# Kernel tuning notes

Hardware: AMD Instinct MI355X
Metric: run time of the kernel (lower is better)

The kernel has to match this reference:

```python
import jax, jax.numpy as jnp
import numpy as np

N_NODES = 100000


def _gcn_layer(x, W, b, src, dst, n):
    # PyG GCNConv: x' = D^-1/2 (A+I) D^-1/2 (x W) + b, with self-loops added.
    x = x @ W  # [N, out]
    loop = jnp.arange(n, dtype=src.dtype)
    src_f = jnp.concatenate([src, loop])
    dst_f = jnp.concatenate([dst, loop])
    deg = jax.ops.segment_sum(jnp.ones_like(dst_f, dtype=x.dtype), dst_f, num_segments=n)
    dinv = jnp.where(deg > 0, jax.lax.rsqrt(deg), 0.0)
    norm = dinv[src_f] * dinv[dst_f]  # [E+N]
    msgs = x[src_f] * norm[:, None]   # gather + scale
    out = jax.ops.segment_sum(msgs, dst_f, num_segments=n)
    return out + b


def setup_inputs() -> dict:
    key = jax.random.key(0)
    ks = jax.random.split(key, 16)
    inputFeatures = jax.random.normal(ks[0], (N_NODES, 64), dtype=jnp.float32)
    edge_index = jax.random.randint(ks[1], (2, 1000000), 0, N_NODES, dtype=jnp.int64)

    def lin(k, fan_in, fan_out):
        s = 1.0 / np.sqrt(fan_in)
        return jax.random.uniform(k, (fan_in, fan_out), jnp.float32, -s, s)

    return {
        "inputFeatures": inputFeatures,
        "W1": lin(ks[2], 64, 100), "b1": jnp.zeros((100,), jnp.float32),
        "W2": lin(ks[3], 100, 50), "b2": jnp.zeros((50,), jnp.float32),
        "W3": lin(ks[4], 50, 25), "b3": jnp.zeros((25,), jnp.float32),
        "Wl1": lin(ks[5], 25, 25), "bl1": jnp.zeros((25,), jnp.float32),
        "Wl2": lin(ks[6], 25, 10), "bl2": jnp.zeros((10,), jnp.float32),
        "Wl3": lin(ks[7], 10, 1), "bl3": jnp.zeros((1,), jnp.float32),
        "edge_index": edge_index,
    }


def reference(inputFeatures, W1, b1, W2, b2, W3, b3, Wl1, bl1, Wl2, bl2, Wl3, bl3, edge_index):
    src, dst = edge_index[0], edge_index[1]
    n = inputFeatures.shape[0]
    x = jax.nn.relu(_gcn_layer(inputFeatures, W1, b1, src, dst, n))
    x = jax.nn.relu(_gcn_layer(x, W2, b2, src, dst, n))
    x = jax.nn.relu(_gcn_layer(x, W3, b3, src, dst, n))
    x = jax.nn.relu(x @ Wl1 + bl1)
    x = jax.nn.relu(x @ Wl2 + bl2)
    x = jax.nn.relu(x @ Wl3 + bl3)
    return x  # [N, 1]
```

## Files before the change

kernel.cpp:

```cpp
#include <hip/hip_runtime.h>
#include <hip/hip_fp16.h>
#include <cstdint>

constexpr int BSHIFT = 9;
constexpr int NBUCK  = 256;
constexpr int BUCKET_CAP = 6144;

struct alignas(16) H8 { __half2 a, b, c, d; };
struct alignas(8)  H4 { __half2 a, b; };

typedef _Float16 f16x8 __attribute__((ext_vector_type(8)));
typedef float    f32x4 __attribute__((ext_vector_type(4)));

__device__ __forceinline__ float4 add4(float4 a, float4 b) {
    return make_float4(a.x + b.x, a.y + b.y, a.z + b.z, a.w + b.w);
}
__device__ __forceinline__ float4 mul4s(float4 a, float s) {
    return make_float4(a.x * s, a.y * s, a.z * s, a.w * s);
}
__device__ __forceinline__ void acc_h8(float4& A0, float4& A1, const H8 v, float s) {
    float2 f0 = __half22float2(v.a), f1 = __half22float2(v.b);
    float2 f2 = __half22float2(v.c), f3 = __half22float2(v.d);
    A0.x = fmaf(f0.x, s, A0.x); A0.y = fmaf(f0.y, s, A0.y);
    A0.z = fmaf(f1.x, s, A0.z); A0.w = fmaf(f1.y, s, A0.w);
    A1.x = fmaf(f2.x, s, A1.x); A1.y = fmaf(f2.y, s, A1.y);
    A1.z = fmaf(f3.x, s, A1.z); A1.w = fmaf(f3.y, s, A1.w);
}


constexpr int EPT = 16;
__global__ __launch_bounds__(256) void partition_pack(
    const int* __restrict__ src, const int* __restrict__ dst,
    int* __restrict__ bucketCur, int* __restrict__ pairs, int ne, int nEdgeBlocks,
    const float* __restrict__ W1, const float* __restrict__ W2,
    const float* __restrict__ W3,
    __half* __restrict__ P1, __half* __restrict__ P2, __half* __restrict__ P3) {
    if (blockIdx.x == (unsigned)nEdgeBlocks) {
        int t = threadIdx.x;
        for (int i = t; i < 7 * 2 * 64 * 8; i += 256) {
            int j = i & 7, lane = (i >> 3) & 63, f = i >> 9;
            int mt = f >> 1, kf = f & 1;
            int k = kf * 32 + (lane >> 4) * 8 + j;
            int m = mt * 16 + (lane & 15);
            P1[i] = __float2half_rn(m < 100 ? W1[k * 100 + m] : 0.0f);
        }
        for (int i = t; i < 4 * 4 * 64 * 8; i += 256) {
            int j = i & 7, lane = (i >> 3) & 63, f = i >> 9;
            int mt = f >> 2, kf = f & 3;
            int k = kf * 32 + (lane >> 4) * 8 + j;
            int m = mt * 16 + (lane & 15);
            P2[i] = __float2half_rn((k < 100 && m < 50) ? W2[k * 50 + m] : 0.0f);
        }
        for (int i = t; i < 2 * 2 * 64 * 8; i += 256) {
            int j = i & 7, lane = (i >> 3) & 63, f = i >> 9;
            int mt = f >> 1, kf = f & 1;
            int k = kf * 32 + (lane >> 4) * 8 + j;
            int m = mt * 16 + (lane & 15);
            P3[i] = __float2half_rn((k < 50 && m < 25) ? W3[k * 25 + m] : 0.0f);
        }
        return;
    }
    __shared__ int lcnt[NBUCK];
    __shared__ int lbase[NBUCK];
    int base = blockIdx.x * (256 * EPT);
    if (threadIdx.x < NBUCK) lcnt[threadIdx.x] = 0;
    __syncthreads();
    int2 ed[EPT];
    int  rnk[EPT];
#pragma unroll
    for (int j = 0; j < EPT; ++j) {
        int e = base + j * 256 + threadIdx.x;
        if (e < ne) {
            int d = dst[e];
            ed[j] = make_int2(src[e], d);
            rnk[j] = atomicAdd(&lcnt[d >> BSHIFT], 1);
        } else {
            ed[j].y = -1;
        }
    }
    __syncthreads();
    if (threadIdx.x < NBUCK) {
        int c = lcnt[threadIdx.x];
        lbase[threadIdx.x] = c ? atomicAdd(&bucketCur[threadIdx.x], c) : 0;
    }
    __syncthreads();
#pragma unroll
    for (int j = 0; j < EPT; ++j) {
        if (ed[j].y >= 0) {
            int b = ed[j].y >> BSHIFT;
            int p = lbase[b] + rnk[j];
            if (p < BUCKET_CAP)
                pairs[(size_t)b * BUCKET_CAP + p] =
                    (ed[j].x << BSHIFT) | (ed[j].y & ((1 << BSHIFT) - 1));
        }
    }
}

__global__ __launch_bounds__(256) void bucket_csr_scan(
    const int* __restrict__ pairs, const int* __restrict__ bucketCnt,
    int* __restrict__ offs, float* __restrict__ dinv, int* __restrict__ csr,
    int n, int ne, int nbuckets) {
    constexpr int BN = 1 << BSHIFT;
    __shared__ int hist[BN];
    __shared__ int cur[BN];
    __shared__ int tmp[256];
    __shared__ int baseS;
    int b = blockIdx.x;
    int t = threadIdx.x;

    int c = (t < (unsigned)nbuckets) ? bucketCnt[t] : 0;
    tmp[t] = c;
    __syncthreads();
    for (int off = 1; off < 256; off <<= 1) {
        int v = (t >= (unsigned)off) ? tmp[t - off] : 0;
        __syncthreads();
        tmp[t] += v;
        __syncthreads();
    }
    if (t == 0) {
        baseS = b ? tmp[b - 1] : 0;
        if (b == 0) offs[n] = ne;
    }
    __syncthreads();
    int base = baseS;
    int cnt  = bucketCnt[b];
    const int* pb = pairs + (size_t)b * BUCKET_CAP;
    int nodeLo = b << BSHIFT;

    hist[t] = 0;
    hist[t + 256] = 0;
    __syncthreads();
    for (int e = t; e < cnt; e += 256)
        atomicAdd(&hist[pb[e] & (BN - 1)], 1);
    __syncthreads();

    int l0 = 2 * t, l1 = l0 + 1;
    int h0 = hist[l0], h1 = hist[l1];
    tmp[t] = h0 + h1;
    __syncthreads();
    for (int off = 1; off < 256; off <<= 1) {
        int v = (t >= (unsigned)off) ? tmp[t - off] : 0;
        __syncthreads();
        tmp[t] += v;
        __syncthreads();
    }
    int e0 = tmp[t] - (h0 + h1);
    int e1 = e0 + h0;
    int g0 = nodeLo + l0, g1 = nodeLo + l1;
    if (g0 < n) { offs[g0] = base + e0; dinv[g0] = rsqrtf((float)(h0 + 1)); }
    if (g1 < n) { offs[g1] = base + e1; dinv[g1] = rsqrtf((float)(h1 + 1)); }
    cur[l0] = e0;
    cur[l1] = e1;
    __syncthreads();

    for (int e = t; e < cnt; e += 256) {
        int p = pb[e];
        int pos = atomicAdd(&cur[p & (BN - 1)], 1);
        csr[base + pos] = ((unsigned)p) >> BSHIFT;
    }
}

__global__ void cvt_scale_f32_f16(const float* __restrict__ x, const float* __restrict__ dinv,
                                  __half* __restrict__ o, int n4) {
    int i = blockIdx.x * blockDim.x + threadIdx.x;
    if (i < n4) {
        float dv = dinv[i >> 4];
        float4 v = ((const float4*)x)[i];
        H4 h;
        h.a = __floats2half2_rn(v.x * dv, v.y * dv);
        h.b = __floats2half2_rn(v.z * dv, v.w * dv);
        ((H4*)o)[i] = h;
    }
}

constexpr int XSP = 72;
constexpr int HPS = 136;
__global__ __launch_bounds__(256, 4) void agg1gemm12(
    const __half* __restrict__ x, const int* __restrict__ offs,
    const int* __restrict__ csr, const float* __restrict__ dinv,
    const __half* __restrict__ P1, const float* __restrict__ b1,
    const __half* __restrict__ P2, __half* __restrict__ out, int n) {
    __shared__ alignas(16) _Float16 Xs[64 * XSP];
    __shared__ alignas(16) _Float16 Hs[64 * HPS];
    int tid = threadIdx.x, lane = tid & 63, w = tid >> 6;
    int lg = lane >> 4, lr = lane & 15;
    int blockBase = blockIdx.x * 64;

    for (int i = tid; i < 64 * 2; i += 256) {
        f16x8 zz = {};
        *(f16x8*)&Hs[(i >> 1) * HPS + 112 + (i & 1) * 8] = zz;
    }

    int f0 = (lane & 7) * 8;
#pragma unroll
    for (int p = 0; p < 2; ++p) {
        int nl = w * 16 + p * 8 + (lane >> 3);
        int node = blockBase + nl;
        float4 z4 = make_float4(0.f, 0.f, 0.f, 0.f);
        float4 a00 = z4, a01 = z4, a10 = z4, a11 = z4, a20 = z4, a21 = z4, a30 = z4, a31 = z4;
        float dv = 0.0f;
        if (node < n) {
            dv = dinv[node];
            H8 sv = *(const H8*)&x[(size_t)node * 64 + f0];
            acc_h8(a00, a01, sv, 1.0f);
            int e0 = offs[node], e1 = offs[node + 1];
            int e = e0;
            for (; e + 4 <= e1; e += 4) {
                int i0 = csr[e], i1 = csr[e + 1], i2 = csr[e + 2], i3 = csr[e + 3];
                H8 v0 = *(const H8*)&x[(size_t)i0 * 64 + f0];
                H8 v1 = *(const H8*)&x[(size_t)i1 * 64 + f0];
                H8 v2 = *(const H8*)&x[(size_t)i2 * 64 + f0];
                H8 v3 = *(const H8*)&x[(size_t)i3 * 64 + f0];
                acc_h8(a00, a01, v0, 1.0f);
                acc_h8(a10, a11, v1, 1.0f);
                acc_h8(a20, a21, v2, 1.0f);
                acc_h8(a30, a31, v3, 1.0f);
            }
            for (; e < e1; ++e) {
                H8 v = *(const H8*)&x[(size_t)csr[e] * 64 + f0];
                acc_h8(a00, a01, v, 1.0f);
            }
        }
        float4 A0 = add4(add4(a00, a10), add4(a20, a30));
        float4 A1 = add4(add4(a01, a11), add4(a21, a31));
        A0 = mul4s(A0, dv);
        A1 = mul4s(A1, dv);
        H8 h;
        h.a = __floats2half2_rn(A0.x, A0.y);
        h.b = __floats2half2_rn(A0.z, A0.w);
        h.c = __floats2half2_rn(A1.x, A1.y);
        h.d = __floats2half2_rn(A1.z, A1.w);
        *(H8*)&Xs[nl * XSP + f0] = h;
    }
    __syncthreads();

    const f16x8* P1v = (const f16x8*)P1;
    float b1v[7];
#pragma unroll
    for (int mt = 0; mt < 7; ++mt) {
        int m = mt * 16 + lr;
        b1v[mt] = (m < 100) ? b1[m] : 0.0f;
    }
    {
        int rowL = w * 16 + lr;
        f16x8 a0 = *(const f16x8*)&Xs[rowL * XSP + lg * 8];
        f16x8 a1 = *(const f16x8*)&Xs[rowL * XSP + 32 + lg * 8];
        int hbase = w * 16;
#pragma unroll
        for (int mt = 0; mt < 7; ++mt) {
            f16x8 w0 = P1v[(mt * 2 + 0) * 64 + lane];
            f16x8 w1 = P1v[(mt * 2 + 1) * 64 + lane];
            f32x4 acc = {};
            acc = __builtin_amdgcn_mfma_f32_16x16x32_f16(a0, w0, acc, 0, 0, 0);
            acc = __builtin_amdgcn_mfma_f32_16x16x32_f16(a1, w1, acc, 0, 0, 0);
            int col = mt * 16 + lr;
#pragma unroll
            for (int i = 0; i < 4; ++i) {
                int rloc = hbase + lg * 4 + i;
                Hs[rloc * HPS + col] = (_Float16)fmaxf(acc[i] + b1v[mt], 0.0f);
            }
        }
    }
    __syncthreads();

    const f16x8* P2v = (const f16x8*)P2;
#pragma unroll
    for (int mt = 0; mt < 4; ++mt) {
        f16x8 w0 = P2v[(mt * 4 + 0) * 64 + lane];
        f16x8 w1 = P2v[(mt * 4 + 1) * 64 + lane];
        f16x8 w2 = P2v[(mt * 4 + 2) * 64 + lane];
        f16x8 w3 = P2v[(mt * 4 + 3) * 64 + lane];
        int lbase = w * 16;
        const _Float16* hrow = &Hs[(size_t)(lbase + lr) * HPS];
        f16x8 a0 = *(const f16x8*)&hrow[lg * 8];
        f16x8 a1 = *(const f16x8*)&hrow[32 + lg * 8];
        f16x8 a2 = *(const f16x8*)&hrow[64 + lg * 8];
        f16x8 a3 = *(const f16x8*)&hrow[96 + lg * 8];
        f32x4 acc = {};
        acc = __builtin_amdgcn_mfma_f32_16x16x32_f16(a0, w0, acc, 0, 0, 0);
        acc = __builtin_amdgcn_mfma_f32_16x16x32_f16(a1, w1, acc, 0, 0, 0);
        acc = __builtin_amdgcn_mfma_f32_16x16x32_f16(a2, w2, acc, 0, 0, 0);
        acc = __builtin_amdgcn_mfma_f32_16x16x32_f16(a3, w3, acc, 0, 0, 0);
        int col = mt * 16 + lr;
#pragma unroll
        for (int i = 0; i < 4; ++i) {
            int node = blockBase + lbase + lg * 4 + i;
            if (node < n)
                out[(size_t)node * 64 + col] = __float2half_rn(acc[i] * dinv[node]);
        }
    }
}

constexpr int YP = 72;
__global__ __launch_bounds__(256) void agg2g3(
    const __half* __restrict__ s, const int* __restrict__ offs,
    const int* __restrict__ csr, const float* __restrict__ dinv,
    const float* __restrict__ b2, const __half* __restrict__ P3,
    __half* __restrict__ out, int n) {
    constexpr int MH = 50, SH = 64;
    __shared__ alignas(16) _Float16 Ys[32 * YP];
    int tid = threadIdx.x, lane = tid & 63, w = tid >> 6;
    int lg = lane >> 4, lr = lane & 15;
    int blockBase = blockIdx.x * 32;

    int nodeL = tid >> 3;
    int f0 = (tid & 7) * 8;
    int node = blockBase + nodeL;
    float v[8] = {0.f, 0.f, 0.f, 0.f, 0.f, 0.f, 0.f, 0.f};
    if (node < n && f0 < 56) {
        float dv = dinv[node];
        float4 z4 = make_float4(0.f, 0.f, 0.f, 0.f);
        float4 a00 = z4, a01 = z4, a10 = z4, a11 = z4, a20 = z4, a21 = z4, a30 = z4, a31 = z4;
        {
            H8 sv = *(const H8*)&s[(size_t)node * SH + f0];
            acc_h8(a00, a01, sv, 1.0f);
        }
        int e0 = offs[node], e1 = offs[node + 1];
        int e = e0;
        for (; e + 4 <= e1; e += 4) {
            int i0 = csr[e], i1 = csr[e + 1], i2 = csr[e + 2], i3 = csr[e + 3];
            H8 v0 = *(const H8*)&s[(size_t)i0 * SH + f0];
            H8 v1 = *(const H8*)&s[(size_t)i1 * SH + f0];
            H8 v2 = *(const H8*)&s[(size_t)i2 * SH + f0];
            H8 v3 = *(const H8*)&s[(size_t)i3 * SH + f0];
            acc_h8(a00, a01, v0, 1.0f);
            acc_h8(a10, a11, v1, 1.0f);
            acc_h8(a20, a21, v2, 1.0f);
            acc_h8(a30, a31, v3, 1.0f);
        }
        for (; e < e1; ++e) {
            H8 vv = *(const H8*)&s[(size_t)csr[e] * SH + f0];
            acc_h8(a00, a01, vv, 1.0f);
        }
        float4 A0 = add4(add4(a00, a10), add4(a20, a30));
        float4 A1 = add4(add4(a01, a11), add4(a21, a31));
        float vr[8] = {A0.x, A0.y, A0.z, A0.w, A1.x, A1.y, A1.z, A1.w};
#pragma unroll
        for (int i = 0; i < 8; ++i)
            v[i] = (f0 + i < MH) ? fmaxf(dv * vr[i] + b2[f0 + i], 0.0f) : 0.0f;
    }
    {
        H8 h;
        h.a = __floats2half2_rn(v[0], v[1]);
        h.b = __floats2half2_rn(v[2], v[3]);
        h.c = __floats2half2_rn(v[4], v[5]);
        h.d = __floats2half2_rn(v[6], v[7]);
        *(H8*)&Ys[nodeL * YP + f0] = h;
    }
    __syncthreads();

    int rt = w >> 1, mt = w & 1;
    const f16x8* P3v = (const f16x8*)P3;
    f16x8 w0 = P3v[(mt * 2 + 0) * 64 + lane];
    f16x8 w1 = P3v[(mt * 2 + 1) * 64 + lane];
    int rowL = rt * 16 + lr;
    f16x8 a0 = *(const f16x8*)&Ys[rowL * YP + lg * 8];
    f16x8 a1 = *(const f16x8*)&Ys[rowL * YP + 32 + lg * 8];
    f32x4 acc = {};
    acc = __builtin_amdgcn_mfma_f32_16x16x32_f16(a0, w0, acc, 0, 0, 0);
    acc = __builtin_amdgcn_mfma_f32_16x16x32_f16(a1, w1, acc, 0, 0, 0);
    int col = mt * 16 + lr;
#pragma unroll
    for (int i = 0; i < 4; ++i) {
        int nd = blockBase + rt * 16 + lg * 4 + i;
        if (nd < n)
            out[(size_t)nd * 32 + col] = __float2half_rn(acc[i] * dinv[nd]);
    }
}

__global__ __launch_bounds__(256) void agg3_mlp_h(
    const __half* __restrict__ s, const int* __restrict__ offs,
    const int* __restrict__ csr, const float* __restrict__ dinv,
    const float* __restrict__ bg,
    const float* __restrict__ Wl1, const float* __restrict__ bl1,
    const float* __restrict__ Wl2, const float* __restrict__ bl2,
    const float* __restrict__ Wl3, const float* __restrict__ bl3,
    float* __restrict__ out, int n) {
    constexpr int MH = 25, SH = 32, LPN = 4;
    __shared__ float W1s[625], W2s[250], W3s[10], b1s[25], b2s[10];
    __shared__ float accs[64 * 26];
    __shared__ float b3s;

    for (int i = threadIdx.x; i < 625; i += 256) W1s[i] = Wl1[i];
    for (int i = threadIdx.x; i < 250; i += 256) W2s[i] = Wl2[i];
    if (threadIdx.x < 10) { W3s[threadIdx.x] = Wl3[threadIdx.x]; b2s[threadIdx.x] = bl2[threadIdx.x]; }
    if (threadIdx.x < 25) b1s[threadIdx.x] = bl1[threadIdx.x];
    if (threadIdx.x == 0) b3s = bl3[0];

    int lane = threadIdx.x % LPN;
    int nl   = threadIdx.x / LPN;
    int node = blockIdx.x * 64 + nl;
    int f0 = lane * 8;

    if (node < n && f0 < MH) {
        float dv = dinv[node];
        float4 z = make_float4(0.f, 0.f, 0.f, 0.f);
        float4 a00 = z, a01 = z, a10 = z, a11 = z, a20 = z, a21 = z, a30 = z, a31 = z;
        {
            H8 sv = *(const H8*)&s[(size_t)node * SH + f0];
            acc_h8(a00, a01, sv, 1.0f);
        }
        int e0 = offs[node], e1 = offs[node + 1];
        int e = e0;
        for (; e + 4 <= e1; e += 4) {
            int i0 = csr[e], i1 = csr[e + 1], i2 = csr[e + 2], i3 = csr[e + 3];
            H8 v0 = *(const H8*)&s[(size_t)i0 * SH + f0];
            H8 v1 = *(const H8*)&s[(size_t)i1 * SH + f0];
            H8 v2 = *(const H8*)&s[(size_t)i2 * SH + f0];
            H8 v3 = *(const H8*)&s[(size_t)i3 * SH + f0];
            acc_h8(a00, a01, v0, 1.0f);
            acc_h8(a10, a11, v1, 1.0f);
            acc_h8(a20, a21, v2, 1.0f);
            acc_h8(a30, a31, v3, 1.0f);
        }
        for (; e < e1; ++e) {
            H8 v = *(const H8*)&s[(size_t)csr[e] * SH + f0];
            acc_h8(a00, a01, v, 1.0f);
        }
        float4 A0 = add4(add4(a00, a10), add4(a20, a30));
        float4 A1 = add4(add4(a01, a11), add4(a21, a31));
        float v[8] = {A0.x, A0.y, A0.z, A0.w, A1.x, A1.y, A1.z, A1.w};
#pragma unroll
        for (int i = 0; i < 8; ++i)
            if (f0 + i < MH)
                accs[nl * 26 + f0 + i] = fmaxf(dv * v[i] + bg[f0 + i], 0.0f);
    }
    __syncthreads();

    if (threadIdx.x < 64) {
        int nd = blockIdx.x * 64 + threadIdx.x;
        if (nd < n) {
            const float* xr = &accs[threadIdx.x * 26];
            float h1[25];
#pragma unroll
            for (int m = 0; m < 25; ++m) {
                float a = b1s[m];
#pragma unroll
                for (int k = 0; k < 25; ++k) a = fmaf(xr[k], W1s[k * 25 + m], a);
                h1[m] = fmaxf(a, 0.0f);
            }
            float h2[10];
#pragma unroll
            for (int m = 0; m < 10; ++m) {
                float a = b2s[m];
#pragma unroll
                for (int k = 0; k < 25; ++k) a = fmaf(h1[k], W2s[k * 10 + m], a);
                h2[m] = fmaxf(a, 0.0f);
            }
            float a = b3s;
#pragma unroll
            for (int k = 0; k < 10; ++k) a = fmaf(h2[k], W3s[k], a);
            out[nd] = fmaxf(a, 0.0f);
        }
    }
}


extern "C" void kernel_launch(void* const* d_in, const int* in_sizes, int n_in,
                              void* d_out, int out_size, void* d_ws, size_t ws_size,
                              hipStream_t stream) {
    const float* x0  = (const float*)d_in[0];
    const float* W1  = (const float*)d_in[1];
    const float* b1  = (const float*)d_in[2];
    const float* W2  = (const float*)d_in[3];
    const float* b2  = (const float*)d_in[4];
    const float* W3  = (const float*)d_in[5];
    const float* b3  = (const float*)d_in[6];
    const float* Wl1 = (const float*)d_in[7];
    const float* bl1 = (const float*)d_in[8];
    const float* Wl2 = (const float*)d_in[9];
    const float* bl2 = (const float*)d_in[10];
    const float* Wl3 = (const float*)d_in[11];
    const float* bl3 = (const float*)d_in[12];
    const int*   edge = (const int*)d_in[13];

    int n  = in_sizes[0] / 64;
    int ne = in_sizes[13] / 2;
    const int* esrc = edge;
    const int* edst = edge + ne;

    char* ws = (char*)d_ws;
    auto alloc = [&](size_t bytes) {
        char* p = ws;
        ws += (bytes + 255) & ~(size_t)255;
        return p;
    };
    int*    offs       = (int*)alloc((size_t)(n + 1) * 4);
    int*    bucketCur  = (int*)alloc(NBUCK * 4);
    int*    csr        = (int*)alloc((size_t)ne * 4);
    float*  dinv       = (float*)alloc((size_t)n * 4);
    __half* x0h        = (__half*)alloc((size_t)n * 64 * 2);
    __half* bufDh      = (__half*)alloc((size_t)n * 64 * 2);
    __half* bufCh      = (__half*)alloc((size_t)n * 32 * 2);
    __half* P1         = (__half*)alloc(7 * 2 * 64 * 8 * 2);
    __half* P2         = (__half*)alloc(4 * 4 * 64 * 8 * 2);
    __half* P3         = (__half*)alloc(2 * 2 * 64 * 8 * 2);
    int*    pairs = (int*)bufDh;
    (void)ws_size; (void)n_in; (void)out_size;

    int nbuckets = (n + (1 << BSHIFT) - 1) >> BSHIFT;
    int nchunk   = (ne + 256 * EPT - 1) / (256 * EPT);

    hipMemsetAsync(bucketCur, 0, NBUCK * 4, stream);
    partition_pack<<<nchunk + 1, 256, 0, stream>>>(
        esrc, edst, bucketCur, pairs, ne, nchunk, W1, W2, W3, P1, P2, P3);
    bucket_csr_scan<<<nbuckets, 256, 0, stream>>>(
        pairs, bucketCur, offs, dinv, csr, n, ne, nbuckets);

    cvt_scale_f32_f16<<<(n * 16 + 255) / 256, 256, 0, stream>>>(x0, dinv, x0h, n * 16);

    agg1gemm12<<<(n + 63) / 64, 256, 0, stream>>>(
        x0h, offs, csr, dinv, P1, b1, P2, bufDh, n);

    agg2g3<<<(n + 31) / 32, 256, 0, stream>>>(
        bufDh, offs, csr, dinv, b2, P3, bufCh, n);

    agg3_mlp_h<<<(n + 63) / 64, 256, 0, stream>>>(
        bufCh, offs, csr, dinv, b3, Wl1, bl1, Wl2, bl2, Wl3, bl3, (float*)d_out, n);
}
```

Baseline: 230.8 us.

## Fuse input fp16 conversion into CSR build and parallelize MLP head

```diff
diff --git a/kernel.cpp b/kernel.cpp
--- a/kernel.cpp
+++ b/kernel.cpp
@@ -5,6 +5,7 @@
 constexpr int BSHIFT = 9;
 constexpr int NBUCK  = 256;
 constexpr int BUCKET_CAP = 6144;
+constexpr int BN = 1 << BSHIFT;
 
 struct alignas(16) H8 { __half2 a, b, c, d; };
 struct alignas(8)  H4 { __half2 a, b; };
@@ -91,16 +92,16 @@
             int p = lbase[b] + rnk[j];
             if (p < BUCKET_CAP)
                 pairs[(size_t)b * BUCKET_CAP + p] =
-                    (ed[j].x << BSHIFT) | (ed[j].y & ((1 << BSHIFT) - 1));
-        }
-    }
-}
-
-__global__ __launch_bounds__(256) void bucket_csr_scan(
+                    (ed[j].x << BSHIFT) | (ed[j].y & (BN - 1));
+        }
+    }
+}
+
+__global__ __launch_bounds__(256) void bucket_csr_cvt(
     const int* __restrict__ pairs, const int* __restrict__ bucketCnt,
     int* __restrict__ offs, float* __restrict__ dinv, int* __restrict__ csr,
+    const float* __restrict__ x0, __half* __restrict__ x0h,
     int n, int ne, int nbuckets) {
-    constexpr int BN = 1 << BSHIFT;
     __shared__ int hist[BN];
     __shared__ int cur[BN];
     __shared__ int tmp[256];
@@ -147,8 +148,12 @@
     int e0 = tmp[t] - (h0 + h1);
     int e1 = e0 + h0;
     int g0 = nodeLo + l0, g1 = nodeLo + l1;
-    if (g0 < n) { offs[g0] = base + e0; dinv[g0] = rsqrtf((float)(h0 + 1)); }
-    if (g1 < n) { offs[g1] = base + e1; dinv[g1] = rsqrtf((float)(h1 + 1)); }
+    float dv0 = rsqrtf((float)(h0 + 1));
+    float dv1 = rsqrtf((float)(h1 + 1));
+    if (g0 < n) { offs[g0] = base + e0; dinv[g0] = dv0; }
+    if (g1 < n) { offs[g1] = base + e1; dinv[g1] = dv1; }
+    hist[l0] = __float_as_int(dv0);
+    hist[l1] = __float_as_int(dv1);
     cur[l0] = e0;
     cur[l1] = e1;
     __syncthreads();
@@ -158,18 +163,20 @@
         int pos = atomicAdd(&cur[p & (BN - 1)], 1);
         csr[base + pos] = ((unsigned)p) >> BSHIFT;
     }
-}
-
-__global__ void cvt_scale_f32_f16(const float* __restrict__ x, const float* __restrict__ dinv,
-                                  __half* __restrict__ o, int n4) {
-    int i = blockIdx.x * blockDim.x + threadIdx.x;
-    if (i < n4) {
-        float dv = dinv[i >> 4];
-        float4 v = ((const float4*)x)[i];
+    __syncthreads();
+
+    int nloc = n - nodeLo;
+    if (nloc > BN) nloc = BN;
+    int cnt16 = nloc * 16;
+    for (int i = t; i < cnt16; i += 256) {
+        int r = i >> 4;
+        float dv = __int_as_float(hist[r]);
+        size_t gi = (size_t)(nodeLo + r) * 16 + (i & 15);
+        float4 v = ((const float4*)x0)[gi];
         H4 h;
         h.a = __floats2half2_rn(v.x * dv, v.y * dv);
         h.b = __floats2half2_rn(v.z * dv, v.w * dv);
-        ((H4*)o)[i] = h;
+        ((H4*)x0h)[gi] = h;
     }
 }
 
@@ -297,7 +304,6 @@
     const int* __restrict__ csr, const float* __restrict__ dinv,
     const float* __restrict__ b2, const __half* __restrict__ P3,
     __half* __restrict__ out, int n) {
-    constexpr int MH = 50, SH = 64;
     __shared__ alignas(16) _Float16 Ys[32 * YP];
     int tid = threadIdx.x, lane = tid & 63, w = tid >> 6;
     int lg = lane >> 4, lr = lane & 15;
@@ -312,24 +318,24 @@
         float4 z4 = make_float4(0.f, 0.f, 0.f, 0.f);
         float4 a00 = z4, a01 = z4, a10 = z4, a11 = z4, a20 = z4, a21 = z4, a30 = z4, a31 = z4;
         {
-            H8 sv = *(const H8*)&s[(size_t)node * SH + f0];
+            H8 sv = *(const H8*)&s[(size_t)node * 64 + f0];
             acc_h8(a00, a01, sv, 1.0f);
         }
         int e0 = offs[node], e1 = offs[node + 1];
         int e = e0;
         for (; e + 4 <= e1; e += 4) {
             int i0 = csr[e], i1 = csr[e + 1], i2 = csr[e + 2], i3 = csr[e + 3];
-            H8 v0 = *(const H8*)&s[(size_t)i0 * SH + f0];
-            H8 v1 = *(const H8*)&s[(size_t)i1 * SH + f0];
-            H8 v2 = *(const H8*)&s[(size_t)i2 * SH + f0];
-            H8 v3 = *(const H8*)&s[(size_t)i3 * SH + f0];
+            H8 v0 = *(const H8*)&s[(size_t)i0 * 64 + f0];
+            H8 v1 = *(const H8*)&s[(size_t)i1 * 64 + f0];
+            H8 v2 = *(const H8*)&s[(size_t)i2 * 64 + f0];
+            H8 v3 = *(const H8*)&s[(size_t)i3 * 64 + f0];
             acc_h8(a00, a01, v0, 1.0f);
             acc_h8(a10, a11, v1, 1.0f);
             acc_h8(a20, a21, v2, 1.0f);
             acc_h8(a30, a31, v3, 1.0f);
         }
         for (; e < e1; ++e) {
-            H8 vv = *(const H8*)&s[(size_t)csr[e] * SH + f0];
+            H8 vv = *(const H8*)&s[(size_t)csr[e] * 64 + f0];
             acc_h8(a00, a01, vv, 1.0f);
         }
         float4 A0 = add4(add4(a00, a10), add4(a20, a30));
@@ -337,7 +343,7 @@
         float vr[8] = {A0.x, A0.y, A0.z, A0.w, A1.x, A1.y, A1.z, A1.w};
 #pragma unroll
         for (int i = 0; i < 8; ++i)
-            v[i] = (f0 + i < MH) ? fmaxf(dv * vr[i] + b2[f0 + i], 0.0f) : 0.0f;
+            v[i] = (f0 + i < 50) ? fmaxf(dv * vr[i] + b2[f0 + i], 0.0f) : 0.0f;
     }
     {
         H8 h;
@@ -376,9 +382,10 @@
     const float* __restrict__ Wl2, const float* __restrict__ bl2,
     const float* __restrict__ Wl3, const float* __restrict__ bl3,
     float* __restrict__ out, int n) {
-    constexpr int MH = 25, SH = 32, LPN = 4;
     __shared__ float W1s[625], W2s[250], W3s[10], b1s[25], b2s[10];
     __shared__ float accs[64 * 26];
+    __shared__ float h1s[64 * 25];
+    __shared__ float h2s[64 * 12];
     __shared__ float b3s;
 
     for (int i = threadIdx.x; i < 625; i += 256) W1s[i] = Wl1[i];
@@ -387,34 +394,34 @@
     if (threadIdx.x < 25) b1s[threadIdx.x] = bl1[threadIdx.x];
     if (threadIdx.x == 0) b3s = bl3[0];
 
-    int lane = threadIdx.x % LPN;
-    int nl   = threadIdx.x / LPN;
+    int lane = threadIdx.x & 3;
+    int nl   = threadIdx.x >> 2;
     int node = blockIdx.x * 64 + nl;
     int f0 = lane * 8;
 
-    if (node < n && f0 < MH) {
+    if (node < n && f0 < 25) {
         float dv = dinv[node];
-        float4 z = make_float4(0.f, 0.f, 0.f, 0.f);
-        float4 a00 = z, a01 = z, a10 = z, a11 = z, a20 = z, a21 = z, a30 = z, a31 = z;
+        float4 z4 = make_float4(0.f, 0.f, 0.f, 0.f);
+        float4 a00 = z4, a01 = z4, a10 = z4, a11 = z4, a20 = z4, a21 = z4, a30 = z4, a31 = z4;
         {
-            H8 sv = *(const H8*)&s[(size_t)node * SH + f0];
+            H8 sv = *(const H8*)&s[(size_t)node * 32 + f0];
             acc_h8(a00, a01, sv, 1.0f);
         }
         int e0 = offs[node], e1 = offs[node + 1];
         int e = e0;
         for (; e + 4 <= e1; e += 4) {
             int i0 = csr[e], i1 = csr[e + 1], i2 = csr[e + 2], i3 = csr[e + 3];
-            H8 v0 = *(const H8*)&s[(size_t)i0 * SH + f0];
-            H8 v1 = *(const H8*)&s[(size_t)i1 * SH + f0];
-            H8 v2 = *(const H8*)&s[(size_t)i2 * SH + f0];
-            H8 v3 = *(const H8*)&s[(size_t)i3 * SH + f0];
+            H8 v0 = *(const H8*)&s[(size_t)i0 * 32 + f0];
+            H8 v1 = *(const H8*)&s[(size_t)i1 * 32 + f0];
+            H8 v2 = *(const H8*)&s[(size_t)i2 * 32 + f0];
+            H8 v3 = *(const H8*)&s[(size_t)i3 * 32 + f0];
             acc_h8(a00, a01, v0, 1.0f);
             acc_h8(a10, a11, v1, 1.0f);
             acc_h8(a20, a21, v2, 1.0f);
             acc_h8(a30, a31, v3, 1.0f);
         }
         for (; e < e1; ++e) {
-            H8 v = *(const H8*)&s[(size_t)csr[e] * SH + f0];
+            H8 v = *(const H8*)&s[(size_t)csr[e] * 32 + f0];
             acc_h8(a00, a01, v, 1.0f);
         }
         float4 A0 = add4(add4(a00, a10), add4(a20, a30));
@@ -422,36 +429,39 @@
         float v[8] = {A0.x, A0.y, A0.z, A0.w, A1.x, A1.y, A1.z, A1.w};
 #pragma unroll
         for (int i = 0; i < 8; ++i)
-            if (f0 + i < MH)
+            if (f0 + i < 25)
                 accs[nl * 26 + f0 + i] = fmaxf(dv * v[i] + bg[f0 + i], 0.0f);
     }
     __syncthreads();
 
-    if (threadIdx.x < 64) {
-        int nd = blockIdx.x * 64 + threadIdx.x;
-        if (nd < n) {
-            const float* xr = &accs[threadIdx.x * 26];
-            float h1[25];
-#pragma unroll
-            for (int m = 0; m < 25; ++m) {
-                float a = b1s[m];
-#pragma unroll
-                for (int k = 0; k < 25; ++k) a = fmaf(xr[k], W1s[k * 25 + m], a);
-                h1[m] = fmaxf(a, 0.0f);
-            }
-            float h2[10];
-#pragma unroll
-            for (int m = 0; m < 10; ++m) {
-                float a = b2s[m];
-#pragma unroll
-                for (int k = 0; k < 25; ++k) a = fmaf(h1[k], W2s[k * 10 + m], a);
-                h2[m] = fmaxf(a, 0.0f);
-            }
-            float a = b3s;
-#pragma unroll
-            for (int k = 0; k < 10; ++k) a = fmaf(h2[k], W3s[k], a);
-            out[nd] = fmaxf(a, 0.0f);
-        }
+    if (node < n) {
+        const float* xr = &accs[nl * 26];
+        for (int m = lane; m < 25; m += 4) {
+            float acc = b1s[m];
+#pragma unroll
+            for (int k = 0; k < 25; ++k) acc = fmaf(xr[k], W1s[k * 25 + m], acc);
+            h1s[nl * 25 + m] = fmaxf(acc, 0.0f);
+        }
+    }
+    __syncthreads();
+
+    if (node < n) {
+        const float* hr = &h1s[nl * 25];
+        for (int m = lane; m < 10; m += 4) {
+            float acc = b2s[m];
+#pragma unroll
+            for (int k = 0; k < 25; ++k) acc = fmaf(hr[k], W2s[k * 10 + m], acc);
+            h2s[nl * 12 + m] = fmaxf(acc, 0.0f);
+        }
+    }
+    __syncthreads();
+
+    if (node < n && lane == 0) {
+        const float* h2 = &h2s[nl * 12];
+        float acc = b3s;
+#pragma unroll
+        for (int k = 0; k < 10; ++k) acc = fmaf(h2[k], W3s[k], acc);
+        out[node] = fmaxf(acc, 0.0f);
     }
 }
 
@@ -504,10 +514,8 @@
     hipMemsetAsync(bucketCur, 0, NBUCK * 4, stream);
     partition_pack<<<nchunk + 1, 256, 0, stream>>>(
         esrc, edst, bucketCur, pairs, ne, nchunk, W1, W2, W3, P1, P2, P3);
-    bucket_csr_scan<<<nbuckets, 256, 0, stream>>>(
-        pairs, bucketCur, offs, dinv, csr, n, ne, nbuckets);
-
-    cvt_scale_f32_f16<<<(n * 16 + 255) / 256, 256, 0, stream>>>(x0, dinv, x0h, n * 16);
+    bucket_csr_cvt<<<nbuckets, 256, 0, stream>>>(
+        pairs, bucketCur, offs, dinv, csr, x0, x0h, n, ne, nbuckets);
 
     agg1gemm12<<<(n + 63) / 64, 256, 0, stream>>>(
         x0h, offs, csr, dinv, P1, b1, P2, bufDh, n);
```

After: 238.9 us. +3.5%, slower.

## Sort nodes by in-degree into a permutation to balance aggregation warps

Applied to the files above, without the earlier changes.

```diff
diff --git a/kernel.cpp b/kernel.cpp
--- a/kernel.cpp
+++ b/kernel.cpp
@@ -5,6 +5,7 @@
 constexpr int BSHIFT = 9;
 constexpr int NBUCK  = 256;
 constexpr int BUCKET_CAP = 6144;
+constexpr int BN = 1 << BSHIFT;
 
 struct alignas(16) H8 { __half2 a, b, c, d; };
 struct alignas(8)  H4 { __half2 a, b; };
@@ -91,7 +92,7 @@
             int p = lbase[b] + rnk[j];
             if (p < BUCKET_CAP)
                 pairs[(size_t)b * BUCKET_CAP + p] =
-                    (ed[j].x << BSHIFT) | (ed[j].y & ((1 << BSHIFT) - 1));
+                    (ed[j].x << BSHIFT) | (ed[j].y & (BN - 1));
         }
     }
 }
@@ -99,11 +100,11 @@
 __global__ __launch_bounds__(256) void bucket_csr_scan(
     const int* __restrict__ pairs, const int* __restrict__ bucketCnt,
     int* __restrict__ offs, float* __restrict__ dinv, int* __restrict__ csr,
-    int n, int ne, int nbuckets) {
-    constexpr int BN = 1 << BSHIFT;
+    int* __restrict__ binCount, int n, int ne, int nbuckets) {
     __shared__ int hist[BN];
     __shared__ int cur[BN];
     __shared__ int tmp[256];
+    __shared__ int binLoc[64];
     __shared__ int baseS;
     int b = blockIdx.x;
     int t = threadIdx.x;
@@ -136,6 +137,7 @@
 
     int l0 = 2 * t, l1 = l0 + 1;
     int h0 = hist[l0], h1 = hist[l1];
+    if (t < 64) binLoc[t] = 0;
     tmp[t] = h0 + h1;
     __syncthreads();
     for (int off = 1; off < 256; off <<= 1) {
@@ -147,17 +149,49 @@
     int e0 = tmp[t] - (h0 + h1);
     int e1 = e0 + h0;
     int g0 = nodeLo + l0, g1 = nodeLo + l1;
-    if (g0 < n) { offs[g0] = base + e0; dinv[g0] = rsqrtf((float)(h0 + 1)); }
-    if (g1 < n) { offs[g1] = base + e1; dinv[g1] = rsqrtf((float)(h1 + 1)); }
+    if (g0 < n) {
+        offs[g0] = base + e0; dinv[g0] = rsqrtf((float)(h0 + 1));
+        atomicAdd(&binLoc[h0 < 63 ? h0 : 63], 1);
+    }
+    if (g1 < n) {
+        offs[g1] = base + e1; dinv[g1] = rsqrtf((float)(h1 + 1));
+        atomicAdd(&binLoc[h1 < 63 ? h1 : 63], 1);
+    }
     cur[l0] = e0;
     cur[l1] = e1;
     __syncthreads();
+    if (t < 64 && binLoc[t]) atomicAdd(&binCount[t], binLoc[t]);
 
     for (int e = t; e < cnt; e += 256) {
         int p = pb[e];
         int pos = atomicAdd(&cur[p & (BN - 1)], 1);
         csr[base + pos] = ((unsigned)p) >> BSHIFT;
     }
+}
+
+__global__ __launch_bounds__(256) void build_perm(
+    const int* __restrict__ offs, const int* __restrict__ binCount,
+    int* __restrict__ binNext, int* __restrict__ perm, int n) {
+    __shared__ int binBase[64];
+    __shared__ int binLoc[64];
+    __shared__ int binResv[64];
+    int b = blockIdx.x, t = threadIdx.x;
+    if (t == 0) {
+        int s = 0;
+        for (int i = 0; i < 64; ++i) { binBase[i] = s; s += binCount[i]; }
+    }
+    if (t < 64) binLoc[t] = 0;
+    __syncthreads();
+    int nodeLo = b << BSHIFT;
+    int g0 = nodeLo + 2 * t, g1 = g0 + 1;
+    int d0 = 0, d1 = 0, r0 = 0, r1 = 0;
+    if (g0 < n) { int d = offs[g0 + 1] - offs[g0]; d0 = d < 63 ? d : 63; r0 = atomicAdd(&binLoc[d0], 1); }
+    if (g1 < n) { int d = offs[g1 + 1] - offs[g1]; d1 = d < 63 ? d : 63; r1 = atomicAdd(&binLoc[d1], 1); }
+    __syncthreads();
+    if (t < 64) binResv[t] = binLoc[t] ? atomicAdd(&binNext[t], binLoc[t]) : 0;
+    __syncthreads();
+    if (g0 < n) perm[binBase[d0] + binResv[d0] + r0] = g0;
+    if (g1 < n) perm[binBase[d1] + binResv[d1] + r1] = g1;
 }
 
 __global__ void cvt_scale_f32_f16(const float* __restrict__ x, const float* __restrict__ dinv,
@@ -178,10 +212,12 @@
 __global__ __launch_bounds__(256, 4) void agg1gemm12(
     const __half* __restrict__ x, const int* __restrict__ offs,
     const int* __restrict__ csr, const float* __restrict__ dinv,
+    const int* __restrict__ perm,
     const __half* __restrict__ P1, const float* __restrict__ b1,
     const __half* __restrict__ P2, __half* __restrict__ out, int n) {
     __shared__ alignas(16) _Float16 Xs[64 * XSP];
     __shared__ alignas(16) _Float16 Hs[64 * HPS];
+    __shared__ int permS[64];
     int tid = threadIdx.x, lane = tid & 63, w = tid >> 6;
     int lg = lane >> 4, lr = lane & 15;
     int blockBase = blockIdx.x * 64;
@@ -190,16 +226,21 @@
         f16x8 zz = {};
         *(f16x8*)&Hs[(i >> 1) * HPS + 112 + (i & 1) * 8] = zz;
     }
+    if (tid < 64) {
+        int idx = blockBase + tid;
+        permS[tid] = (idx < n) ? perm[idx] : -1;
+    }
+    __syncthreads();
 
     int f0 = (lane & 7) * 8;
 #pragma unroll
     for (int p = 0; p < 2; ++p) {
         int nl = w * 16 + p * 8 + (lane >> 3);
-        int node = blockBase + nl;
+        int node = permS[nl];
         float4 z4 = make_float4(0.f, 0.f, 0.f, 0.f);
         float4 a00 = z4, a01 = z4, a10 = z4, a11 = z4, a20 = z4, a21 = z4, a30 = z4, a31 = z4;
         float dv = 0.0f;
-        if (node < n) {
+        if (node >= 0) {
             dv = dinv[node];
             H8 sv = *(const H8*)&x[(size_t)node * 64 + f0];
             acc_h8(a00, a01, sv, 1.0f);
@@ -284,8 +325,8 @@
         int col = mt * 16 + lr;
 #pragma unroll
         for (int i = 0; i < 4; ++i) {
-            int node = blockBase + lbase + lg * 4 + i;
-            if (node < n)
+            int node = permS[lbase + lg * 4 + i];
+            if (node >= 0)
                 out[(size_t)node * 64 + col] = __float2half_rn(acc[i] * dinv[node]);
         }
     }
@@ -295,41 +336,48 @@
 __global__ __launch_bounds__(256) void agg2g3(
     const __half* __restrict__ s, const int* __restrict__ offs,
     const int* __restrict__ csr, const float* __restrict__ dinv,
+    const int* __restrict__ perm,
     const float* __restrict__ b2, const __half* __restrict__ P3,
     __half* __restrict__ out, int n) {
-    constexpr int MH = 50, SH = 64;
     __shared__ alignas(16) _Float16 Ys[32 * YP];
+    __shared__ int permS[32];
     int tid = threadIdx.x, lane = tid & 63, w = tid >> 6;
     int lg = lane >> 4, lr = lane & 15;
     int blockBase = blockIdx.x * 32;
 
+    if (tid < 32) {
+        int idx = blockBase + tid;
+        permS[tid] = (idx < n) ? perm[idx] : -1;
+    }
+    __syncthreads();
+
     int nodeL = tid >> 3;
     int f0 = (tid & 7) * 8;
-    int node = blockBase + nodeL;
+    int node = permS[nodeL];
     float v[8] = {0.f, 0.f, 0.f, 0.f, 0.f, 0.f, 0.f, 0.f};
-    if (node < n && f0 < 56) {
+    if (node >= 0 && f0 < 56) {
         float dv = dinv[node];
         float4 z4 = make_float4(0.f, 0.f, 0.f, 0.f);
         float4 a00 = z4, a01 = z4, a10 = z4, a11 = z4, a20 = z4, a21 = z4, a30 = z4, a31 = z4;
         {
-            H8 sv = *(const H8*)&s[(size_t)node * SH + f0];
+            H8 sv = *(const H8*)&s[(size_t)node * 64 + f0];
             acc_h8(a00, a01, sv, 1.0f);
         }
         int e0 = offs[node], e1 = offs[node + 1];
         int e = e0;
         for (; e + 4 <= e1; e += 4) {
             int i0 = csr[e], i1 = csr[e + 1], i2 = csr[e + 2], i3 = csr[e + 3];
-            H8 v0 = *(const H8*)&s[(size_t)i0 * SH + f0];
-            H8 v1 = *(const H8*)&s[(size_t)i1 * SH + f0];
-            H8 v2 = *(const H8*)&s[(size_t)i2 * SH + f0];
-            H8 v3 = *(const H8*)&s[(size_t)i3 * SH + f0];
+            H8 v0 = *(const H8*)&s[(size_t)i0 * 64 + f0];
+            H8 v1 = *(const H8*)&s[(size_t)i1 * 64 + f0];
+            H8 v2 = *(const H8*)&s[(size_t)i2 * 64 + f0];
+            H8 v3 = *(const H8*)&s[(size_t)i3 * 64 + f0];
             acc_h8(a00, a01, v0, 1.0f);
             acc_h8(a10, a11, v1, 1.0f);
             acc_h8(a20, a21, v2, 1.0f);
             acc_h8(a30, a31, v3, 1.0f);
         }
         for (; e < e1; ++e) {
-            H8 vv = *(const H8*)&s[(size_t)csr[e] * SH + f0];
+            H8 vv = *(const H8*)&s[(size_t)csr[e] * 64 + f0];
             acc_h8(a00, a01, vv, 1.0f);
         }
         float4 A0 = add4(add4(a00, a10), add4(a20, a30));
@@ -337,7 +385,7 @@
         float vr[8] = {A0.x, A0.y, A0.z, A0.w, A1.x, A1.y, A1.z, A1.w};
 #pragma unroll
         for (int i = 0; i < 8; ++i)
-            v[i] = (f0 + i < MH) ? fmaxf(dv * vr[i] + b2[f0 + i], 0.0f) : 0.0f;
+            v[i] = (f0 + i < 50) ? fmaxf(dv * vr[i] + b2[f0 + i], 0.0f) : 0.0f;
     }
     {
         H8 h;
@@ -362,8 +410,8 @@
     int col = mt * 16 + lr;
 #pragma unroll
     for (int i = 0; i < 4; ++i) {
-        int nd = blockBase + rt * 16 + lg * 4 + i;
-        if (nd < n)
+        int nd = permS[rt * 16 + lg * 4 + i];
+        if (nd >= 0)
             out[(size_t)nd * 32 + col] = __float2half_rn(acc[i] * dinv[nd]);
     }
 }
@@ -371,14 +419,16 @@
 __global__ __launch_bounds__(256) void agg3_mlp_h(
     const __half* __restrict__ s, const int* __restrict__ offs,
     const int* __restrict__ csr, const float* __restrict__ dinv,
+    const int* __restrict__ perm,
     const float* __restrict__ bg,
     const float* __restrict__ Wl1, const float* __restrict__ bl1,
     const float* __restrict__ Wl2, const float* __restrict__ bl2,
     const float* __restrict__ Wl3, const float* __restrict__ bl3,
     float* __restrict__ out, int n) {
-    constexpr int MH = 25, SH = 32, LPN = 4;
+    constexpr int LPN = 4;
     __shared__ float W1s[625], W2s[250], W3s[10], b1s[25], b2s[10];
     __shared__ float accs[64 * 26];
+    __shared__ int permS[64];
     __shared__ float b3s;
 
     for (int i = threadIdx.x; i < 625; i += 256) W1s[i] = Wl1[i];
@@ -386,35 +436,40 @@
     if (threadIdx.x < 10) { W3s[threadIdx.x] = Wl3[threadIdx.x]; b2s[threadIdx.x] = bl2[threadIdx.x]; }
     if (threadIdx.x < 25) b1s[threadIdx.x] = bl1[threadIdx.x];
     if (threadIdx.x == 0) b3s = bl3[0];
+    if (threadIdx.x < 64) {
+        int idx = blockIdx.x * 64 + threadIdx.x;
+        permS[threadIdx.x] = (idx < n) ? perm[idx] : -1;
+    }
+    __syncthreads();
 
     int lane = threadIdx.x % LPN;
     int nl   = threadIdx.x / LPN;
-    int node = blockIdx.x * 64 + nl;
+    int node = permS[nl];
     int f0 = lane * 8;
 
-    if (node < n && f0 < MH) {
+    if (node >= 0 && f0 < 25) {
         float dv = dinv[node];
-        float4 z = make_float4(0.f, 0.f, 0.f, 0.f);
-        float4 a00 = z, a01 = z, a10 = z, a11 = z, a20 = z, a21 = z, a30 = z, a31 = z;
+        float4 z4 = make_float4(0.f, 0.f, 0.f, 0.f);
+        float4 a00 = z4, a01 = z4, a10 = z4, a11 = z4, a20 = z4, a21 = z4, a30 = z4, a31 = z4;
         {
-            H8 sv = *(const H8*)&s[(size_t)node * SH + f0];
+            H8 sv = *(const H8*)&s[(size_t)node * 32 + f0];
             acc_h8(a00, a01, sv, 1.0f);
         }
         int e0 = offs[node], e1 = offs[node + 1];
         int e = e0;
         for (; e + 4 <= e1; e += 4) {
             int i0 = csr[e], i1 = csr[e + 1], i2 = csr[e + 2], i3 = csr[e + 3];
-            H8 v0 = *(const H8*)&s[(size_t)i0 * SH + f0];
-            H8 v1 = *(const H8*)&s[(size_t)i1 * SH + f0];
-            H8 v2 = *(const H8*)&s[(size_t)i2 * SH + f0];
-            H8 v3 = *(const H8*)&s[(size_t)i3 * SH + f0];
+            H8 v0 = *(const H8*)&s[(size_t)i0 * 32 + f0];
+            H8 v1 = *(const H8*)&s[(size_t)i1 * 32 + f0];
+            H8 v2 = *(const H8*)&s[(size_t)i2 * 32 + f0];
+            H8 v3 = *(const H8*)&s[(size_t)i3 * 32 + f0];
             acc_h8(a00, a01, v0, 1.0f);
             acc_h8(a10, a11, v1, 1.0f);
             acc_h8(a20, a21, v2, 1.0f);
             acc_h8(a30, a31, v3, 1.0f);
         }
         for (; e < e1; ++e) {
-            H8 v = *(const H8*)&s[(size_t)csr[e] * SH + f0];
+            H8 v = *(const H8*)&s[(size_t)csr[e] * 32 + f0];
             acc_h8(a00, a01, v, 1.0f);
         }
         float4 A0 = add4(add4(a00, a10), add4(a20, a30));
@@ -422,14 +477,14 @@
         float v[8] = {A0.x, A0.y, A0.z, A0.w, A1.x, A1.y, A1.z, A1.w};
 #pragma unroll
         for (int i = 0; i < 8; ++i)
-            if (f0 + i < MH)
+            if (f0 + i < 25)
                 accs[nl * 26 + f0 + i] = fmaxf(dv * v[i] + bg[f0 + i], 0.0f);
     }
     __syncthreads();
 
     if (threadIdx.x < 64) {
-        int nd = blockIdx.x * 64 + threadIdx.x;
-        if (nd < n) {
+        int nd = permS[threadIdx.x];
+        if (nd >= 0) {
             const float* xr = &accs[threadIdx.x * 26];
             float h1[25];
 #pragma unroll
@@ -486,35 +541,40 @@
         return p;
     };
     int*    offs       = (int*)alloc((size_t)(n + 1) * 4);
-    int*    bucketCur  = (int*)alloc(NBUCK * 4);
+    int*    bucketCur  = (int*)alloc((NBUCK + 128) * 4);
     int*    csr        = (int*)alloc((size_t)ne * 4);
     float*  dinv       = (float*)alloc((size_t)n * 4);
+    int*    perm       = (int*)alloc((size_t)n * 4);
     __half* x0h        = (__half*)alloc((size_t)n * 64 * 2);
     __half* bufDh      = (__half*)alloc((size_t)n * 64 * 2);
     __half* bufCh      = (__half*)alloc((size_t)n * 32 * 2);
     __half* P1         = (__half*)alloc(7 * 2 * 64 * 8 * 2);
     __half* P2         = (__half*)alloc(4 * 4 * 64 * 8 * 2);
     __half* P3         = (__half*)alloc(2 * 2 * 64 * 8 * 2);
+    int* binCount = bucketCur + NBUCK;
+    int* binNext  = bucketCur + NBUCK + 64;
     int*    pairs = (int*)bufDh;
     (void)ws_size; (void)n_in; (void)out_size;
 
     int nbuckets = (n + (1 << BSHIFT) - 1) >> BSHIFT;
     int nchunk   = (ne + 256 * EPT - 1) / (256 * EPT);
 
-    hipMemsetAsync(bucketCur, 0, NBUCK * 4, stream);
+    hipMemsetAsync(bucketCur, 0, (NBUCK + 128) * 4, stream);
     partition_pack<<<nchunk + 1, 256, 0, stream>>>(
         esrc, edst, bucketCur, pairs, ne, nchunk, W1, W2, W3, P1, P2, P3);
     bucket_csr_scan<<<nbuckets, 256, 0, stream>>>(
-        pairs, bucketCur, offs, dinv, csr, n, ne, nbuckets);
+        pairs, bucketCur, offs, dinv, csr, binCount, n, ne, nbuckets);
+
+    build_perm<<<nbuckets, 256, 0, stream>>>(offs, binCount, binNext, perm, n);
 
     cvt_scale_f32_f16<<<(n * 16 + 255) / 256, 256, 0, stream>>>(x0, dinv, x0h, n * 16);
 
     agg1gemm12<<<(n + 63) / 64, 256, 0, stream>>>(
-        x0h, offs, csr, dinv, P1, b1, P2, bufDh, n);
+        x0h, offs, csr, dinv, perm, P1, b1, P2, bufDh, n);
 
     agg2g3<<<(n + 31) / 32, 256, 0, stream>>>(
-        bufDh, offs, csr, dinv, b2, P3, bufCh, n);
+        bufDh, offs, csr, dinv, perm, b2, P3, bufCh, n);
 
     agg3_mlp_h<<<(n + 63) / 64, 256, 0, stream>>>(
-        bufCh, offs, csr, dinv, b3, Wl1, bl1, Wl2, bl2, Wl3, bl3, (float*)d_out, n);
-}
+        bufCh, offs, csr, dinv, perm, b3, Wl1, bl1, Wl2, bl2, Wl3, bl3, (float*)d_out, n);
+}
```

Result: slower. 240.6 us (+4.2%).
